# Performance work log

Measured on AMD Instinct MI355X. Metric: run time of the kernel, lower is better.

Reference implementation:

```python
import jax, jax.numpy as jnp
import numpy as np

B, N, DIM = 2, 2048, 2048
H, KVH, HD = 16, 4, 128
N_REP = H // KVH
SCALE = np.float32(HD ** -0.5)


def setup_inputs() -> dict:
    key = jax.random.key(0)
    ks = jax.random.split(key, 5)
    x = jax.random.normal(ks[0], (B, N, DIM), dtype=jnp.float32)
    mask = jnp.tril(jnp.ones((N, N), dtype=jnp.int32))[None, None]  # [1,1,N,N] causal
    Wq = jax.random.normal(ks[1], (DIM, H * HD), dtype=jnp.float32) * (DIM ** -0.5)
    Wk = jax.random.normal(ks[2], (DIM, KVH * HD), dtype=jnp.float32) * (DIM ** -0.5)
    Wv = jax.random.normal(ks[3], (DIM, KVH * HD), dtype=jnp.float32) * (DIM ** -0.5)
    Wo = jax.random.normal(ks[4], (H * HD, DIM), dtype=jnp.float32) * ((H * HD) ** -0.5)
    return {"x": x, "mask": mask, "Wq": Wq, "Wk": Wk, "Wv": Wv, "Wo": Wo}


def reference(x, mask, Wq, Wk, Wv, Wo):
    Bx, Nx, _ = x.shape
    # projections -> [B, heads, N, head_dim]
    q = (x @ Wq).reshape(Bx, Nx, H, HD).transpose(0, 2, 1, 3)
    k = (x @ Wk).reshape(Bx, Nx, KVH, HD).transpose(0, 2, 1, 3)
    v = (x @ Wv).reshape(Bx, Nx, KVH, HD).transpose(0, 2, 1, 3)
    # repeat_interleave KV heads to match query heads (GQA)
    k = jnp.repeat(k, N_REP, axis=1)
    v = jnp.repeat(v, N_REP, axis=1)
    attn = jnp.einsum('bhqd,bhkd->bhqk', q, k) * SCALE
    attn = jnp.where(mask == 0, jnp.float32(-jnp.inf), attn)
    attn = jax.nn.softmax(attn, axis=-1)
    out = jnp.einsum('bhqk,bhkd->bhqd', attn, v)
    out = out.transpose(0, 2, 1, 3).reshape(Bx, Nx, H * HD)
    return out @ Wo
```

## Files before the change

kernel.cpp:

```cpp
#include <hip/hip_runtime.h>
#include <hip/hip_bf16.h>
#include <math.h>

typedef __bf16 bf16;
typedef bf16 bf16x8 __attribute__((ext_vector_type(8)));
typedef bf16 bf16x4v __attribute__((ext_vector_type(4)));
typedef float f32x4 __attribute__((ext_vector_type(4)));

#define GLD16(g, l) __builtin_amdgcn_global_load_lds(                          \
    (__attribute__((address_space(1))) void*)(g),                              \
    (__attribute__((address_space(3))) void*)(l), 16, 0, 0)

#define MFMA16(a, b, c) __builtin_amdgcn_mfma_f32_16x16x32_bf16((a), (b), (c), 0, 0, 0)

#if __has_builtin(__builtin_amdgcn_exp2f)
#define EXP2F(x) __builtin_amdgcn_exp2f(x)
#else
#define EXP2F(x) exp2f(x)
#endif

__device__ __forceinline__ f32x4 shfl_xor4(f32x4 a, int m) {
  f32x4 r;
  #pragma unroll
  for (int i = 0; i < 4; i++) r[i] = __shfl_xor(a[i], m);
  return r;
}

__global__ __launch_bounds__(256) void prep(const float* __restrict__ x,
                                            const float* __restrict__ Wq,
                                            const float* __restrict__ Wk,
                                            const float* __restrict__ Wv,
                                            const float* __restrict__ Wo,
                                            bf16* __restrict__ Xb,
                                            bf16* __restrict__ Wqkvt,
                                            bf16* __restrict__ Wot,
                                            float qscale) {
  const int id = blockIdx.x;
  const int tid = threadIdx.x;
  if (id >= 10240) {
    int i = (id - 10240) * 256 + tid;
    float4 v = ((const float4*)x)[i];
    bf16x4v o;
    o.x = (bf16)v.x; o.y = (bf16)v.y; o.z = (bf16)v.z; o.w = (bf16)v.w;
    ((bf16x4v*)Xb)[i] = o;
    return;
  }
  __shared__ float t[32][33];
  const float* in; bf16* out; int colsIn, outRowOff, bx, by; float scale;
  if (id < 4096)      { in = Wq; out = Wqkvt; colsIn = 2048; outRowOff = 0;    scale = qscale; bx = id & 63;          by = id >> 6; }
  else if (id < 5120) { in = Wk; out = Wqkvt; colsIn = 512;  outRowOff = 2048; scale = 1.0f;   bx = (id - 4096) & 15; by = (id - 4096) >> 4; }
  else if (id < 6144) { in = Wv; out = Wqkvt; colsIn = 512;  outRowOff = 2560; scale = 1.0f;   bx = (id - 5120) & 15; by = (id - 5120) >> 4; }
  else                { in = Wo; out = Wot;   colsIn = 2048; outRowOff = 0;    scale = 1.0f;   bx = (id - 6144) & 63; by = (id - 6144) >> 6; }
  const int c0 = bx * 32, r0 = by * 32;
  const int tx = tid & 31, ty = tid >> 5;
  #pragma unroll
  for (int i = 0; i < 32; i += 8)
    t[ty + i][tx] = in[(size_t)(r0 + ty + i) * colsIn + (c0 + tx)];
  __syncthreads();
  #pragma unroll
  for (int i = 0; i < 32; i += 8)
    out[(size_t)(outRowOff + c0 + ty + i) * 2048 + (r0 + tx)] = (bf16)(t[tx][ty + i] * scale);
}

template <typename OutT>
__global__ __launch_bounds__(256, 2) void gemm_bt(const bf16* __restrict__ A,
                                                  const bf16* __restrict__ Bt,
                                                  OutT* __restrict__ C,
                                                  bf16* __restrict__ Vg,
                                                  int N, int K) {
  __shared__ __attribute__((aligned(16))) bf16 As[128 * 32];
  __shared__ __attribute__((aligned(16))) bf16 Bs[128 * 32];
  const int tid = threadIdx.x;
  const int lane = tid & 63;
  const int wave = tid >> 6;
  const int wm = wave >> 1, wn = wave & 1;
  const int l15 = lane & 15, quad = lane >> 4;
  const int rowBase = blockIdx.y * 128;
  const int colBase = blockIdx.x * 128;

  f32x4 acc[4][4] = {};

  const int cb0 = wave * 64;
  const int c0 = cb0 + lane;
  const int c1 = c0 + 256;
  const bf16* a0 = A + (size_t)(rowBase + (c0 >> 2)) * K + (c0 & 3) * 8;
  const bf16* a1 = A + (size_t)(rowBase + (c1 >> 2)) * K + (c1 & 3) * 8;
  const bf16* b0 = Bt + (size_t)(colBase + (c0 >> 2)) * K + (c0 & 3) * 8;
  const bf16* b1 = Bt + (size_t)(colBase + (c1 >> 2)) * K + (c1 & 3) * 8;
  bf16* lA0 = &As[cb0 * 8];
  bf16* lA1 = &As[(cb0 + 256) * 8];
  bf16* lB0 = &Bs[cb0 * 8];
  bf16* lB1 = &Bs[(cb0 + 256) * 8];

  for (int k0 = 0; k0 < K; k0 += 32) {
    GLD16(a0 + k0, lA0);
    GLD16(a1 + k0, lA1);
    GLD16(b0 + k0, lB0);
    GLD16(b1 + k0, lB1);
    __syncthreads();
    bf16x8 af[4], bfr[4];
    #pragma unroll
    for (int i = 0; i < 4; i++)
      af[i] = *(const bf16x8*)&As[(wm * 64 + i * 16 + l15) * 32 + quad * 8];
    #pragma unroll
    for (int i = 0; i < 4; i++)
      bfr[i] = *(const bf16x8*)&Bs[(wn * 64 + i * 16 + l15) * 32 + quad * 8];
    #pragma unroll
    for (int i = 0; i < 4; i++)
      #pragma unroll
      for (int j = 0; j < 4; j++)
        acc[i][j] = MFMA16(af[i], bfr[j], acc[i][j]);
    __syncthreads();
  }

  if (Vg != nullptr && colBase >= 2560) {
    const int kvh = (colBase - 2560) >> 7;
    #pragma unroll
    for (int i = 0; i < 4; i++) {
      int row = rowBase + wm * 64 + i * 16 + quad * 4;
      int bb = row >> 11;
      int n0 = row & 2047;
      #pragma unroll
      for (int j = 0; j < 4; j++) {
        int d = wn * 64 + j * 16 + l15;
        bf16x4v o;
        #pragma unroll
        for (int r = 0; r < 4; r++) o[r] = (bf16)acc[i][j][r];
        *(bf16x4v*)&Vg[((size_t)(bb * 4 + kvh) * 128 + d) * 2048 + n0] = o;
      }
    }
  } else {
    #pragma unroll
    for (int i = 0; i < 4; i++) {
      int row = rowBase + wm * 64 + i * 16 + quad * 4;
      #pragma unroll
      for (int j = 0; j < 4; j++) {
        int col = colBase + wn * 64 + j * 16 + l15;
        #pragma unroll
        for (int r = 0; r < 4; r++)
          C[(size_t)(row + r) * N + col] = (OutT)acc[i][j][r];
      }
    }
  }
}

#define MASKV (-1e30f)

__device__ const unsigned char BMAP[22] = {
  28, 58, 24, 50, 20, 46, 36, 32,
  62, 59, 54, 51, 47, 42, 55, 63,
  0, 4, 8, 12, 16, 43
};

#define SLOT_F32 16640

__global__ __launch_bounds__(256, 2) void gqa_attn(const bf16* __restrict__ QKV,
                                                   const bf16* __restrict__ Vg,
                                                   bf16* __restrict__ Obf,
                                                   float* __restrict__ Part) {
  __shared__ __attribute__((aligned(16))) bf16 Kl[64 * 128];
  __shared__ __attribute__((aligned(16))) bf16 Vt[128 * 64];
  __shared__ __attribute__((aligned(16))) bf16 Pl[4][32 * 68];

  const int tid = threadIdx.x;
  const int lane = tid & 63;
  const int wave = tid >> 6;
  const int l15 = lane & 15, quad = lane >> 4;

  const int e = BMAP[blockIdx.x >> 5];
  const int bh = blockIdx.x & 31;
  const int qt = e >> 2;
  const int split = (e >> 1) & 1;
  const int half = e & 1;
  const int b = bh >> 4, h = bh & 15, kvh = h >> 2;
  const int q0 = qt * 128;
  const int nkt = 2 * qt + 2;
  const int kt_lo = (split && half) ? (nkt >> 1) : 0;
  const int kt_hi = (split && !half) ? (nkt >> 1) : nkt;

  const size_t rs = 3072;
  const bf16* Qb  = QKV + (size_t)b * 2048 * rs + h * 128;
  const bf16* Kb  = QKV + (size_t)b * 2048 * rs + 2048 + kvh * 128;
  const bf16* Vgb = Vg + (size_t)(b * 4 + kvh) * 128 * 2048;

  bf16x8 qf[2][4];
  #pragma unroll
  for (int mt = 0; mt < 2; mt++) {
    int row = q0 + wave * 32 + mt * 16 + l15;
    #pragma unroll
    for (int ks = 0; ks < 4; ks++)
      qf[mt][ks] = *(const bf16x8*)&Qb[(size_t)row * rs + ks * 32 + quad * 8];
  }

  bf16x8 ones8;
  #pragma unroll
  for (int i = 0; i < 8; i++) ones8[i] = (bf16)1.0f;

  const bf16* kp[4]; const bf16* vp[4];
  bf16* kl[4]; bf16* vl[4];
  #pragma unroll
  for (int t = 0; t < 4; t++) {
    int keyl = wave * 16 + t * 4 + (lane >> 4);
    int ck = (lane & 15) ^ (4 * (t & 1) + (lane >> 4));
    kp[t] = Kb + (size_t)(kt_lo * 64 + keyl) * rs + ck * 8;
    kl[t] = &Kl[(wave * 16 + t * 4) * 128];
    int dl = wave * 32 + t * 8 + (lane >> 3);
    int cv = (lane & 7) ^ (lane >> 3);
    vp[t] = Vgb + (size_t)dl * 2048 + kt_lo * 64 + cv * 8;
    vl[t] = &Vt[(wave * 32 + t * 8) * 64];
  }

  f32x4 oacc[2][8] = {};
  f32x4 lacc[2] = {};
  f32x4 mrow[2];
  #pragma unroll
  for (int mt = 0; mt < 2; mt++)
    #pragma unroll
    for (int r = 0; r < 4; r++) mrow[mt][r] = MASKV;

  const int myrow_hi = q0 + wave * 32 + 31;
  for (int kt = kt_lo; kt < kt_hi; kt++) {
    const int k0 = kt * 64;
    __syncthreads();
    #pragma unroll
    for (int t = 0; t < 4; t++) { GLD16(kp[t], kl[t]); kp[t] += 64 * rs; }
    #pragma unroll
    for (int t = 0; t < 4; t++) { GLD16(vp[t], vl[t]); vp[t] += 64; }
    __syncthreads();

    if (k0 > myrow_hi) continue;

    f32x4 s[2][4] = {};
    #pragma unroll
    for (int ks = 0; ks < 4; ks++) {
      #pragma unroll
      for (int nt = 0; nt < 4; nt++) {
        bf16x8 kf = *(const bf16x8*)&Kl[(nt * 16 + l15) * 128 +
                                        (((ks * 4 + quad) ^ (l15 & 7)) * 8)];
        s[0][nt] = MFMA16(qf[0][ks], kf, s[0][nt]);
        s[1][nt] = MFMA16(qf[1][ks], kf, s[1][nt]);
      }
    }
    if (kt >= nkt - 2) {
      #pragma unroll
      for (int mt = 0; mt < 2; mt++) {
        int rowb = q0 + wave * 32 + mt * 16 + quad * 4;
        #pragma unroll
        for (int nt = 0; nt < 4; nt++) {
          int col = k0 + nt * 16 + l15;
          #pragma unroll
          for (int r = 0; r < 4; r++)
            if (col > rowb + r) s[mt][nt][r] = MASKV;
        }
      }
    }
    #pragma unroll
    for (int mt = 0; mt < 2; mt++) {
      f32x4 mx = s[mt][0];
      #pragma unroll
      for (int nt = 1; nt < 4; nt++)
        #pragma unroll
        for (int r = 0; r < 4; r++) mx[r] = fmaxf(mx[r], s[mt][nt][r]);
      #pragma unroll
      for (int d = 1; d < 16; d <<= 1) {
        f32x4 o = shfl_xor4(mx, d);
        #pragma unroll
        for (int r = 0; r < 4; r++) mx[r] = fmaxf(mx[r], o[r]);
      }
      bool noresc = (mx[0] <= mrow[mt][0] + 8.f) && (mx[1] <= mrow[mt][1] + 8.f) &&
                    (mx[2] <= mrow[mt][2] + 8.f) && (mx[3] <= mrow[mt][3] + 8.f);
      if (!__all(noresc)) {
        f32x4 alpha;
        #pragma unroll
        for (int r = 0; r < 4; r++) {
          float mn = fmaxf(mrow[mt][r], mx[r]);
          alpha[r] = EXP2F(mrow[mt][r] - mn);
          mrow[mt][r] = mn;
        }
        #pragma unroll
        for (int no = 0; no < 8; no++)
          #pragma unroll
          for (int r = 0; r < 4; r++) oacc[mt][no][r] *= alpha[r];
        #pragma unroll
        for (int r = 0; r < 4; r++) lacc[mt][r] *= alpha[r];
      }
      #pragma unroll
      for (int nt = 0; nt < 4; nt++)
        #pragma unroll
        for (int r = 0; r < 4; r++) {
          float p = EXP2F(s[mt][nt][r] - mrow[mt][r]);
          Pl[wave][(mt * 16 + quad * 4 + r) * 68 + nt * 16 + l15] = (bf16)p;
        }
    }
    #pragma unroll
    for (int ks2 = 0; ks2 < 2; ks2++) {
      bf16x8 pf0 = *(const bf16x8*)&Pl[wave][l15 * 68 + ks2 * 32 + quad * 8];
      bf16x8 pf1 = *(const bf16x8*)&Pl[wave][(16 + l15) * 68 + ks2 * 32 + quad * 8];
      lacc[0] = MFMA16(pf0, ones8, lacc[0]);
      lacc[1] = MFMA16(pf1, ones8, lacc[1]);
      #pragma unroll
      for (int no = 0; no < 8; no++) {
        bf16x8 vf = *(const bf16x8*)&Vt[(no * 16 + l15) * 64 +
                                        (((ks2 * 4 + quad) ^ (l15 & 7)) * 8)];
        oacc[0][no] = MFMA16(pf0, vf, oacc[0][no]);
        oacc[1][no] = MFMA16(pf1, vf, oacc[1][no]);
      }
    }
  }

  if (!split) {
    #pragma unroll
    for (int mt = 0; mt < 2; mt++) {
      f32x4 linv;
      #pragma unroll
      for (int r = 0; r < 4; r++) linv[r] = 1.0f / lacc[mt][r];
      int row = q0 + wave * 32 + mt * 16 + quad * 4;
      #pragma unroll
      for (int no = 0; no < 8; no++) {
        int col = h * 128 + no * 16 + l15;
        #pragma unroll
        for (int r = 0; r < 4; r++)
          Obf[(size_t)(b * 2048 + row + r) * 2048 + col] = (bf16)(oacc[mt][no][r] * linv[r]);
      }
    }
  } else {
    const int fidx = bh * 6 + (qt - 10);
    float* slot = Part + (size_t)(fidx * 2 + half) * SLOT_F32;
    #pragma unroll
    for (int mt = 0; mt < 2; mt++) {
      int row = wave * 32 + mt * 16 + quad * 4;
      #pragma unroll
      for (int no = 0; no < 8; no++) {
        int col = no * 16 + l15;
        #pragma unroll
        for (int r = 0; r < 4; r++)
          slot[(row + r) * 128 + col] = oacc[mt][no][r];
      }
    }
    if (l15 == 0) {
      #pragma unroll
      for (int mt = 0; mt < 2; mt++)
        #pragma unroll
        for (int r = 0; r < 4; r++) {
          int row = wave * 32 + mt * 16 + quad * 4 + r;
          slot[16384 + row] = mrow[mt][r];
          slot[16512 + row] = lacc[mt][r];
        }
    }
  }
}

__global__ __launch_bounds__(256) void merge_split(const float* __restrict__ Part,
                                                   bf16* __restrict__ Obf) {
  const int fidx = blockIdx.x;
  const int bh = fidx / 6, qt = 10 + fidx % 6;
  const int b = bh >> 4, h = bh & 15;
  const int tid = threadIdx.x;
  const int cl = (tid & 31) * 4;
  const int r0 = tid >> 5;
  const float* s0 = Part + (size_t)(fidx * 2) * SLOT_F32;
  const float* s1 = s0 + SLOT_F32;
  #pragma unroll
  for (int i = 0; i < 16; i++) {
    int row = r0 + i * 8;
    float m0 = s0[16384 + row], l0 = s0[16512 + row];
    float m1 = s1[16384 + row], l1 = s1[16512 + row];
    float ms = fmaxf(m0, m1);
    float a0 = EXP2F(m0 - ms), a1 = EXP2F(m1 - ms);
    float linv = 1.0f / (l0 * a0 + l1 * a1);
    f32x4 v0 = *(const f32x4*)&s0[row * 128 + cl];
    f32x4 v1 = *(const f32x4*)&s1[row * 128 + cl];
    bf16x4v o;
    #pragma unroll
    for (int r = 0; r < 4; r++) o[r] = (bf16)((v0[r] * a0 + v1[r] * a1) * linv);
    *(bf16x4v*)&Obf[(size_t)(b * 2048 + qt * 128 + row) * 2048 + h * 128 + cl] = o;
  }
}

extern "C" void kernel_launch(void* const* d_in, const int* in_sizes, int n_in,
                              void* d_out, int out_size, void* d_ws, size_t ws_size,
                              hipStream_t stream) {
  const float* x  = (const float*)d_in[0];
  const float* Wq = (const float*)d_in[2];
  const float* Wk = (const float*)d_in[3];
  const float* Wv = (const float*)d_in[4];
  const float* Wo = (const float*)d_in[5];
  float* out = (float*)d_out;

  bf16* Xb    = (bf16*)d_ws;
  bf16* Wqkvt = Xb + 8388608;
  bf16* Wot   = Wqkvt + 6291456;
  bf16* QKV   = Wot + 4194304;
  bf16* Obf   = QKV + 12582912;
  bf16* Vg    = Obf + 8388608;

  float* Part = (float*)d_ws;

  const float qscale = (float)(0.08838834764831845 * 1.4426950408889634);

  prep<<<18432, 256, 0, stream>>>(x, Wq, Wk, Wv, Wo, Xb, Wqkvt, Wot, qscale);
  gemm_bt<bf16><<<dim3(24, 32), 256, 0, stream>>>(Xb, Wqkvt, QKV, Vg, 3072, 2048);
  gqa_attn<<<704, 256, 0, stream>>>(QKV, Vg, Obf, Part);
  merge_split<<<192, 256, 0, stream>>>(Part, Obf);
  gemm_bt<float><<<dim3(16, 32), 256, 0, stream>>>(Obf, Wot, out, (bf16*)nullptr, 2048, 2048);
}
```

Baseline: 318.3 us.

## Load K/V fragments directly from global memory instead of shared LDS tiles

Removes the cooperative global-to-LDS staging of K and V tiles and the two block-wide barriers per key tile, so each wave reads its MFMA fragments straight from global memory (through cache). Each wave also stops its loop at its own causal limit instead of iterating and skipping. This drops barrier stalls and LDS traffic but makes each of the four waves fetch the full K/V tiles separately, raising global/L2 load volume and exposing memory latency without LDS reuse.

```diff
diff --git a/kernel.cpp b/kernel.cpp
--- a/kernel.cpp
+++ b/kernel.cpp
@@ -158,8 +158,6 @@
                                                    const bf16* __restrict__ Vg,
                                                    bf16* __restrict__ Obf,
                                                    float* __restrict__ Part) {
-  __shared__ __attribute__((aligned(16))) bf16 Kl[64 * 128];
-  __shared__ __attribute__((aligned(16))) bf16 Vt[128 * 64];
   __shared__ __attribute__((aligned(16))) bf16 Pl[4][32 * 68];
 
   const int tid = threadIdx.x;
@@ -196,20 +194,6 @@
   #pragma unroll
   for (int i = 0; i < 8; i++) ones8[i] = (bf16)1.0f;
 
-  const bf16* kp[4]; const bf16* vp[4];
-  bf16* kl[4]; bf16* vl[4];
-  #pragma unroll
-  for (int t = 0; t < 4; t++) {
-    int keyl = wave * 16 + t * 4 + (lane >> 4);
-    int ck = (lane & 15) ^ (4 * (t & 1) + (lane >> 4));
-    kp[t] = Kb + (size_t)(kt_lo * 64 + keyl) * rs + ck * 8;
-    kl[t] = &Kl[(wave * 16 + t * 4) * 128];
-    int dl = wave * 32 + t * 8 + (lane >> 3);
-    int cv = (lane & 7) ^ (lane >> 3);
-    vp[t] = Vgb + (size_t)dl * 2048 + kt_lo * 64 + cv * 8;
-    vl[t] = &Vt[(wave * 32 + t * 8) * 64];
-  }
-
   f32x4 oacc[2][8] = {};
   f32x4 lacc[2] = {};
   f32x4 mrow[2];
@@ -219,24 +203,17 @@
     for (int r = 0; r < 4; r++) mrow[mt][r] = MASKV;
 
   const int myrow_hi = q0 + wave * 32 + 31;
-  for (int kt = kt_lo; kt < kt_hi; kt++) {
+  const int kt_hi_w = min(kt_hi, (myrow_hi >> 6) + 1);
+
+  for (int kt = kt_lo; kt < kt_hi_w; kt++) {
     const int k0 = kt * 64;
-    __syncthreads();
-    #pragma unroll
-    for (int t = 0; t < 4; t++) { GLD16(kp[t], kl[t]); kp[t] += 64 * rs; }
-    #pragma unroll
-    for (int t = 0; t < 4; t++) { GLD16(vp[t], vl[t]); vp[t] += 64; }
-    __syncthreads();
-
-    if (k0 > myrow_hi) continue;
 
     f32x4 s[2][4] = {};
     #pragma unroll
     for (int ks = 0; ks < 4; ks++) {
       #pragma unroll
       for (int nt = 0; nt < 4; nt++) {
-        bf16x8 kf = *(const bf16x8*)&Kl[(nt * 16 + l15) * 128 +
-                                        (((ks * 4 + quad) ^ (l15 & 7)) * 8)];
+        bf16x8 kf = *(const bf16x8*)&Kb[(size_t)(k0 + nt * 16 + l15) * rs + (ks * 4 + quad) * 8];
         s[0][nt] = MFMA16(qf[0][ks], kf, s[0][nt]);
         s[1][nt] = MFMA16(qf[1][ks], kf, s[1][nt]);
       }
@@ -300,8 +277,7 @@
       lacc[1] = MFMA16(pf1, ones8, lacc[1]);
       #pragma unroll
       for (int no = 0; no < 8; no++) {
-        bf16x8 vf = *(const bf16x8*)&Vt[(no * 16 + l15) * 64 +
-                                        (((ks2 * 4 + quad) ^ (l15 & 7)) * 8)];
+        bf16x8 vf = *(const bf16x8*)&Vgb[(size_t)(no * 16 + l15) * 2048 + k0 + ks2 * 32 + quad * 8];
         oacc[0][no] = MFMA16(pf0, vf, oacc[0][no]);
         oacc[1][no] = MFMA16(pf1, vf, oacc[1][no]);
       }
```

After: 418.9 us. 31.6% more time.
